# Optimization experiments

Measured on AMD Instinct MI355X. Metric: run time of the kernel, lower is better.

## Reference

```python
import jax, jax.numpy as jnp
import numpy as np

L, B, D = 2048, 8, 1024
EPS = 1e-5


def setup_inputs() -> dict:
    key = jax.random.key(0)
    k1, k2 = jax.random.split(key)
    x = jax.random.normal(k1, (L, B, D), dtype=jnp.float32)
    c = jnp.zeros((B, D), dtype=jnp.float32)
    # w_ufr: Linear(D, 3D); weight init normal(std=0.001), bias zero except
    # the reset-gate third which is filled with 2.0 (per the torch init).
    W = jax.random.normal(k2, (3 * D, D), dtype=jnp.float32) * 0.001
    b = jnp.zeros((3 * D,), dtype=jnp.float32).at[2 * D:].set(2.0)
    gamma = jnp.ones((D,), dtype=jnp.float32)
    beta = jnp.zeros((D,), dtype=jnp.float32)
    return {"x": x, "c": c, "W": W, "b": b, "gamma": gamma, "beta": beta}


def _layernorm(x, gamma, beta):
    mu = jnp.mean(x, axis=-1, keepdims=True)
    var = jnp.var(x, axis=-1, keepdims=True)
    return (x - mu) * jax.lax.rsqrt(var + EPS) * gamma + beta


def reference(x, c, W, b, gamma, beta):
    residual = x
    x_norm = _layernorm(x, gamma, beta)            # [L,B,D]
    ufr = jnp.einsum('lbd,ed->lbe', x_norm, W) + b  # [L,B,3D]
    u, f, r = jnp.split(ufr, 3, axis=-1)
    f_gate = jax.nn.sigmoid(f)
    r_gate = jax.nn.sigmoid(r)

    def step(c_prev, fu):
        f_t, u_t = fu
        c_t = f_t * c_prev + (1.0 - f_t) * u_t
        return c_t, c_t

    last_c, c_stack = jax.lax.scan(step, c, (f_gate, u))  # c_stack: [L,B,D]
    hs = r_gate * jnp.tanh(c_stack) + (1.0 - r_gate) * x_norm
    # dropout is identity in eval mode
    return residual + hs, last_c
```

## Files before the change

kernel.cpp:

```cpp
#include <hip/hip_runtime.h>
#include <hip/hip_bf16.h>

#define L_DIM 2048
#define B_DIM 8
#define D_DIM 1024
#define M_DIM (L_DIM * B_DIM)
#define N_DIM (3 * D_DIM)
#define K_DIM D_DIM
#define BD (B_DIM * D_DIM)
#define NCHUNK 64
#define CLEN (L_DIM / NCHUNK)

typedef __attribute__((ext_vector_type(8))) __bf16 bf16x8;
typedef __attribute__((ext_vector_type(4))) __bf16 bf16x4;
typedef __attribute__((ext_vector_type(4))) float f32x4;

#define GLOAD_LDS16(g, l)                                        \
  __builtin_amdgcn_global_load_lds(                              \
      (const __attribute__((address_space(1))) void*)(g),        \
      (__attribute__((address_space(3))) void*)(l), 16, 0, 0)

__device__ __forceinline__ float sigmoidf_(float v) {
  return 1.0f / (1.0f + __expf(-v));
}

__global__ __launch_bounds__(256) void ln_kernel(
    const float* __restrict__ x, const float* __restrict__ gamma,
    const float* __restrict__ beta, __bf16* __restrict__ xn) {
  const int row = blockIdx.x;
  const int tid = threadIdx.x;
  const float4 v = ((const float4*)(x + (size_t)row * D_DIM))[tid];
  float s  = v.x + v.y + v.z + v.w;
  float ss = v.x * v.x + v.y * v.y + v.z * v.z + v.w * v.w;
  #pragma unroll
  for (int off = 32; off > 0; off >>= 1) {
    s  += __shfl_xor(s, off);
    ss += __shfl_xor(ss, off);
  }
  __shared__ float sb[8];
  const int wid = tid >> 6, lane = tid & 63;
  if (lane == 0) { sb[wid] = s; sb[4 + wid] = ss; }
  __syncthreads();
  const float tot  = sb[0] + sb[1] + sb[2] + sb[3];
  const float tot2 = sb[4] + sb[5] + sb[6] + sb[7];
  const float mu  = tot * (1.0f / D_DIM);
  const float var = tot2 * (1.0f / D_DIM) - mu * mu;
  const float rstd = rsqrtf(var + 1e-5f);
  const float4 g  = ((const float4*)gamma)[tid];
  const float4 bt = ((const float4*)beta)[tid];
  bf16x4 o;
  o[0] = (__bf16)((v.x - mu) * rstd * g.x + bt.x);
  o[1] = (__bf16)((v.y - mu) * rstd * g.y + bt.y);
  o[2] = (__bf16)((v.z - mu) * rstd * g.z + bt.z);
  o[3] = (__bf16)((v.w - mu) * rstd * g.w + bt.w);
  ((bf16x4*)(xn + (size_t)row * D_DIM))[tid] = o;
}

__global__ __launch_bounds__(256) void wconv_kernel(
    const float* __restrict__ W, __bf16* __restrict__ Wb) {
  const size_t i = ((size_t)blockIdx.x * 256 + threadIdx.x) * 4;
  const float4 v = *(const float4*)(W + i);
  bf16x4 o;
  o[0] = (__bf16)v.x; o[1] = (__bf16)v.y; o[2] = (__bf16)v.z; o[3] = (__bf16)v.w;
  *(bf16x4*)(Wb + i) = o;
}

__global__ __launch_bounds__(256) void gemm_kernel(
    const __bf16* __restrict__ A,
    const __bf16* __restrict__ Bm,
    const float* __restrict__ bias,
    __bf16* __restrict__ U, __bf16* __restrict__ FG, __bf16* __restrict__ RG) {
  __shared__ __bf16 lds[17408];
  const int tid = threadIdx.x;
  const int lane = tid & 63;
  const int wid = tid >> 6;
  const int wm = wid >> 1;
  const int wc = wid & 1;

  const int bid0 = blockIdx.x;
  const int bid = (bid0 & 7) * 384 + (bid0 >> 3);
  const int bm = bid / 24, bn = bid % 24;

  const int srow  = tid >> 3;
  const int sslot = (tid & 7) ^ (srow & 7);
  const __bf16* aSrc = A + (size_t)(bm * 128 + srow) * K_DIM + sslot * 8;
  const __bf16* bSrc = Bm + (size_t)(bn * 128 + srow) * K_DIM + sslot * 8;

  const int fr = lane & 15, fk = lane >> 4;
  const int swzbase = fk ^ (fr & 7);
  auto rdA = [&](int kk, int m) {
    return *(const bf16x8*)(lds + (wm * 64 + m * 16 + fr) * 64 +
                            ((kk * 4) ^ swzbase) * 8);
  };
  auto rdB = [&](int kk, int n) {
    return *(const bf16x8*)(lds + 8192 + (wc * 64 + n * 16 + fr) * 64 +
                            ((kk * 4) ^ swzbase) * 8);
  };

  f32x4 acc[4][4] = {};

  #pragma unroll 1
  for (int kt = 0; kt < 16; ++kt) {
    __syncthreads();
    #pragma unroll
    for (int i = 0; i < 4; ++i) {
      GLOAD_LDS16(aSrc + (size_t)(32 * i) * K_DIM + kt * 64,
                  lds + (tid + 256 * i) * 8);
      GLOAD_LDS16(bSrc + (size_t)(32 * i) * K_DIM + kt * 64,
                  lds + 8192 + (tid + 256 * i) * 8);
    }
    __syncthreads();

    #pragma unroll
    for (int kk = 0; kk < 2; ++kk) {
      bf16x8 a[4], b[4];
      #pragma unroll
      for (int m = 0; m < 4; ++m) a[m] = rdA(kk, m);
      #pragma unroll
      for (int n = 0; n < 4; ++n) b[n] = rdB(kk, n);
      __builtin_amdgcn_s_setprio(1);
      #pragma unroll
      for (int m = 0; m < 4; ++m)
        #pragma unroll
        for (int n = 0; n < 4; ++n)
          acc[m][n] = __builtin_amdgcn_mfma_f32_16x16x32_bf16(
              a[m], b[n], acc[m][n], 0, 0, 0);
      __builtin_amdgcn_s_setprio(0);
    }
  }

  const int seg = bn >> 3;
  __bf16* outb = (seg == 0) ? U : ((seg == 1) ? FG : RG);
  const int segcol0 = (bn & 7) * 128;

  float bv[4];
  #pragma unroll
  for (int n = 0; n < 4; ++n)
    bv[n] = bias[seg * 1024 + segcol0 + wc * 64 + n * 16 + fr];

  __syncthreads();
  #pragma unroll
  for (int m = 0; m < 4; ++m)
    #pragma unroll
    for (int n = 0; n < 4; ++n)
      #pragma unroll
      for (int j = 0; j < 4; ++j) {
        float v = acc[m][n][j] + bv[n];
        if (seg != 0) v = sigmoidf_(v);
        lds[(wm * 64 + m * 16 + fk * 4 + j) * 136 + wc * 64 + n * 16 + fr] =
            (__bf16)v;
      }
  __syncthreads();
  const int lrow = tid >> 4;
  const int chunk = tid & 15;
  #pragma unroll
  for (int it = 0; it < 8; ++it) {
    const int r = it * 16 + lrow;
    const bf16x8 val = *(const bf16x8*)(lds + r * 136 + chunk * 8);
    const size_t grow = (size_t)(bm * 128 + r);
    *(bf16x8*)(outb + grow * D_DIM + segcol0 + chunk * 8) = val;
  }
}

__global__ __launch_bounds__(256) void scanA_kernel(
    const __bf16* __restrict__ fg, const __bf16* __restrict__ u,
    float* __restrict__ av) {
  const int ci = blockIdx.x;
  const int bd = blockIdx.y * 256 + threadIdx.x;
  float a = 1.0f, v = 0.0f;
  const size_t base = (size_t)ci * CLEN * BD + bd;
  #pragma unroll 8
  for (int i = 0; i < CLEN; ++i) {
    const size_t idx = base + (size_t)i * BD;
    const float f = (float)fg[idx];
    const float uu = (float)u[idx];
    a *= f;
    v = f * v + (1.0f - f) * uu;
  }
  av[(size_t)ci * BD + bd] = a;
  av[(size_t)NCHUNK * BD + (size_t)ci * BD + bd] = v;
}

__global__ __launch_bounds__(256) void scanB_kernel(
    const float* __restrict__ av, const float* __restrict__ c0,
    float* __restrict__ carries, float* __restrict__ out1) {
  const int bd = blockIdx.x * 256 + threadIdx.x;
  float c = c0[bd];
  #pragma unroll 8
  for (int ci = 0; ci < NCHUNK; ++ci) {
    carries[(size_t)ci * BD + bd] = c;
    c = av[(size_t)ci * BD + bd] * c + av[(size_t)NCHUNK * BD + (size_t)ci * BD + bd];
  }
  out1[bd] = c;
}

__global__ __launch_bounds__(256) void scanC_kernel(
    const __bf16* __restrict__ fg, const __bf16* __restrict__ u,
    const __bf16* __restrict__ rg, const __bf16* __restrict__ xn,
    const float* __restrict__ x, const float* __restrict__ carries,
    float* __restrict__ out0) {
  const int ci = blockIdx.x;
  const int bd = blockIdx.y * 256 + threadIdx.x;
  float c = carries[(size_t)ci * BD + bd];
  const size_t base = (size_t)ci * CLEN * BD + bd;
  #pragma unroll 4
  for (int i = 0; i < CLEN; ++i) {
    const size_t idx = base + (size_t)i * BD;
    const float f = (float)fg[idx];
    const float uu = (float)u[idx];
    c = f * c + (1.0f - f) * uu;
    const float r = (float)rg[idx];
    const float xnv = (float)xn[idx];
    const float hs = r * tanhf(c) + (1.0f - r) * xnv;
    out0[idx] = x[idx] + hs;
  }
}

extern "C" void kernel_launch(void* const* d_in, const int* in_sizes, int n_in,
                              void* d_out, int out_size, void* d_ws,
                              size_t ws_size, hipStream_t stream) {
  const float* x     = (const float*)d_in[0];
  const float* c0    = (const float*)d_in[1];
  const float* W     = (const float*)d_in[2];
  const float* bias  = (const float*)d_in[3];
  const float* gamma = (const float*)d_in[4];
  const float* beta  = (const float*)d_in[5];

  float* out0 = (float*)d_out;
  float* out1 = out0 + (size_t)M_DIM * D_DIM;

  char* ws = (char*)d_ws;
  __bf16* xn = (__bf16*)(ws + 0);
  __bf16* Wb = (__bf16*)(ws + 33554432);
  __bf16* U  = (__bf16*)(ws + 39845888);
  __bf16* FG = (__bf16*)(ws + 73400320);
  __bf16* RG = (__bf16*)(ws + 106954752);
  float* av      = (float*)(ws + 140509184);
  float* carries = (float*)(ws + 144703488);

  ln_kernel<<<M_DIM, 256, 0, stream>>>(x, gamma, beta, xn);
  wconv_kernel<<<(N_DIM * K_DIM / 4) / 256, 256, 0, stream>>>(W, Wb);
  gemm_kernel<<<(M_DIM / 128) * (N_DIM / 128), 256, 0, stream>>>(
      xn, Wb, bias, U, FG, RG);
  scanA_kernel<<<dim3(NCHUNK, BD / 256), 256, 0, stream>>>(FG, U, av);
  scanB_kernel<<<BD / 256, 256, 0, stream>>>(av, c0, carries, out1);
  scanC_kernel<<<dim3(NCHUNK, BD / 256), 256, 0, stream>>>(
      FG, U, RG, xn, x, carries, out0);
}
```

Baseline: 216.0 us.

## Vectorize scan kernels to 8 elements per thread and recompute layernorm in scanC

scanA and scanC now each handle 8 contiguous channels per thread, using 16-byte bf16x8 and float4 loads and stores in place of scalar accesses. scanC also stops reading the bf16 normalized activations. It recomputes them from x using per-row mean and rstd that ln_kernel now writes out. This cuts memory transactions and removes one bf16 read stream, at the cost of 8x fewer threads: scanA and scanC drop to 256 blocks each, which may underfill the GPU and expose latency.

```diff
diff --git a/kernel.cpp b/kernel.cpp
--- a/kernel.cpp
+++ b/kernel.cpp
@@ -26,7 +26,8 @@
 
 __global__ __launch_bounds__(256) void ln_kernel(
     const float* __restrict__ x, const float* __restrict__ gamma,
-    const float* __restrict__ beta, __bf16* __restrict__ xn) {
+    const float* __restrict__ beta, __bf16* __restrict__ xn,
+    float* __restrict__ muA, float* __restrict__ rsA) {
   const int row = blockIdx.x;
   const int tid = threadIdx.x;
   const float4 v = ((const float4*)(x + (size_t)row * D_DIM))[tid];
@@ -46,6 +47,7 @@
   const float mu  = tot * (1.0f / D_DIM);
   const float var = tot2 * (1.0f / D_DIM) - mu * mu;
   const float rstd = rsqrtf(var + 1e-5f);
+  if (tid == 0) { muA[row] = mu; rsA[row] = rstd; }
   const float4 g  = ((const float4*)gamma)[tid];
   const float4 bt = ((const float4*)beta)[tid];
   bf16x4 o;
@@ -166,19 +168,30 @@
     const __bf16* __restrict__ fg, const __bf16* __restrict__ u,
     float* __restrict__ av) {
   const int ci = blockIdx.x;
-  const int bd = blockIdx.y * 256 + threadIdx.x;
-  float a = 1.0f, v = 0.0f;
-  const size_t base = (size_t)ci * CLEN * BD + bd;
-  #pragma unroll 8
+  const int t8 = blockIdx.y * 256 + threadIdx.x;
+  const int bd0 = t8 * 8;
+  float a[8], v[8];
+  #pragma unroll
+  for (int j = 0; j < 8; ++j) { a[j] = 1.0f; v[j] = 0.0f; }
+  const size_t base = (size_t)ci * CLEN * BD + bd0;
+  #pragma unroll 4
   for (int i = 0; i < CLEN; ++i) {
     const size_t idx = base + (size_t)i * BD;
-    const float f = (float)fg[idx];
-    const float uu = (float)u[idx];
-    a *= f;
-    v = f * v + (1.0f - f) * uu;
-  }
-  av[(size_t)ci * BD + bd] = a;
-  av[(size_t)NCHUNK * BD + (size_t)ci * BD + bd] = v;
+    const bf16x8 fv = *(const bf16x8*)(fg + idx);
+    const bf16x8 uv = *(const bf16x8*)(u + idx);
+    #pragma unroll
+    for (int j = 0; j < 8; ++j) {
+      const float f = (float)fv[j];
+      a[j] *= f;
+      v[j] = f * v[j] + (1.0f - f) * (float)uv[j];
+    }
+  }
+  float4* avA = (float4*)(av + (size_t)ci * BD + bd0);
+  float4* avV = (float4*)(av + (size_t)NCHUNK * BD + (size_t)ci * BD + bd0);
+  avA[0] = make_float4(a[0], a[1], a[2], a[3]);
+  avA[1] = make_float4(a[4], a[5], a[6], a[7]);
+  avV[0] = make_float4(v[0], v[1], v[2], v[3]);
+  avV[1] = make_float4(v[4], v[5], v[6], v[7]);
 }
 
 __global__ __launch_bounds__(256) void scanB_kernel(
@@ -196,23 +209,51 @@
 
 __global__ __launch_bounds__(256) void scanC_kernel(
     const __bf16* __restrict__ fg, const __bf16* __restrict__ u,
-    const __bf16* __restrict__ rg, const __bf16* __restrict__ xn,
-    const float* __restrict__ x, const float* __restrict__ carries,
-    float* __restrict__ out0) {
+    const __bf16* __restrict__ rg, const float* __restrict__ x,
+    const float* __restrict__ muA, const float* __restrict__ rsA,
+    const float* __restrict__ gamma, const float* __restrict__ beta,
+    const float* __restrict__ carries, float* __restrict__ out0) {
   const int ci = blockIdx.x;
-  const int bd = blockIdx.y * 256 + threadIdx.x;
-  float c = carries[(size_t)ci * BD + bd];
-  const size_t base = (size_t)ci * CLEN * BD + bd;
-  #pragma unroll 4
+  const int t8 = blockIdx.y * 256 + threadIdx.x;
+  const int bd0 = t8 * 8;
+  const int b = bd0 >> 10;
+  const int d0 = bd0 & 1023;
+
+  float g[8], be[8], c[8];
+  #pragma unroll
+  for (int j = 0; j < 8; ++j) { g[j] = gamma[d0 + j]; be[j] = beta[d0 + j]; }
+  {
+    const float4* cp = (const float4*)(carries + (size_t)ci * BD + bd0);
+    const float4 c0v = cp[0], c1v = cp[1];
+    c[0] = c0v.x; c[1] = c0v.y; c[2] = c0v.z; c[3] = c0v.w;
+    c[4] = c1v.x; c[5] = c1v.y; c[6] = c1v.z; c[7] = c1v.w;
+  }
+
+  const size_t base = (size_t)ci * CLEN * BD + bd0;
+  #pragma unroll 2
   for (int i = 0; i < CLEN; ++i) {
     const size_t idx = base + (size_t)i * BD;
-    const float f = (float)fg[idx];
-    const float uu = (float)u[idx];
-    c = f * c + (1.0f - f) * uu;
-    const float r = (float)rg[idx];
-    const float xnv = (float)xn[idx];
-    const float hs = r * tanhf(c) + (1.0f - r) * xnv;
-    out0[idx] = x[idx] + hs;
+    const int row = (ci * CLEN + i) * B_DIM + b;
+    const float mu = muA[row], rs = rsA[row];
+    const bf16x8 fv = *(const bf16x8*)(fg + idx);
+    const bf16x8 uv = *(const bf16x8*)(u + idx);
+    const bf16x8 rv = *(const bf16x8*)(rg + idx);
+    const float4* xp = (const float4*)(x + idx);
+    const float4 x0 = xp[0], x1 = xp[1];
+    const float xs[8] = {x0.x, x0.y, x0.z, x0.w, x1.x, x1.y, x1.z, x1.w};
+    float os[8];
+    #pragma unroll
+    for (int j = 0; j < 8; ++j) {
+      const float f = (float)fv[j];
+      c[j] = f * c[j] + (1.0f - f) * (float)uv[j];
+      const float r = (float)rv[j];
+      const float xn = (xs[j] - mu) * rs * g[j] + be[j];
+      const float hs = r * tanhf(c[j]) + (1.0f - r) * xn;
+      os[j] = xs[j] + hs;
+    }
+    float4* op = (float4*)(out0 + idx);
+    op[0] = make_float4(os[0], os[1], os[2], os[3]);
+    op[1] = make_float4(os[4], os[5], os[6], os[7]);
   }
 }
 
@@ -237,13 +278,15 @@
   __bf16* RG = (__bf16*)(ws + 106954752);
   float* av      = (float*)(ws + 140509184);
   float* carries = (float*)(ws + 144703488);
-
-  ln_kernel<<<M_DIM, 256, 0, stream>>>(x, gamma, beta, xn);
+  float* muA     = (float*)(ws + 146800640);
+  float* rsA     = (float*)(ws + 146866176);
+
+  ln_kernel<<<M_DIM, 256, 0, stream>>>(x, gamma, beta, xn, muA, rsA);
   wconv_kernel<<<(N_DIM * K_DIM / 4) / 256, 256, 0, stream>>>(W, Wb);
   gemm_kernel<<<(M_DIM / 128) * (N_DIM / 128), 256, 0, stream>>>(
       xn, Wb, bias, U, FG, RG);
-  scanA_kernel<<<dim3(NCHUNK, BD / 256), 256, 0, stream>>>(FG, U, av);
+  scanA_kernel<<<dim3(NCHUNK, BD / 8 / 256), 256, 0, stream>>>(FG, U, av);
   scanB_kernel<<<BD / 256, 256, 0, stream>>>(av, c0, carries, out1);
-  scanC_kernel<<<dim3(NCHUNK, BD / 256), 256, 0, stream>>>(
-      FG, U, RG, xn, x, carries, out0);
-}
+  scanC_kernel<<<dim3(NCHUNK, BD / 8 / 256), 256, 0, stream>>>(
+      FG, U, RG, x, muA, rsA, gamma, beta, carries, out0);
+}
```

New measurement: 216.4 us (median of 2 runs). Within noise of the previous version (+0.2%).
